# Kernel tuning notes

Hardware: AMD Instinct MI355X
Metric: run time of the kernel (lower is better)

The kernel has to match this reference:

```python
import jax, jax.numpy as jnp
import numpy as np

WS = (17, 5, 1)
NT = 23  # 17+5+1 tokens across levels
TABLE_ROWS = (2 * WS[0] - 1) * (2 * WS[0] - 1)  # 1089


def _rel_index():
    cs = []
    for i, w in enumerate(WS):
        c = np.arange(w, dtype=np.float32) - w // 2
        if i < len(WS) - 1:
            c = c * WS[0] / w  # rescale coarser levels to finest grid
        cs.append(c)
    c = np.concatenate(cs)  # [23]
    return (c[:, None] - c[None, :]) + (WS[0] - 1)  # [23,23] float

REL_IDX = jnp.asarray(_rel_index())


def _avgpool1d(x):
    # AvgPool1d(kernel=2, stride=2, padding=1, count_include_pad=False) on last axis (odd L)
    return jnp.concatenate([x[..., :1], (x[..., 1::2] + x[..., 2::2]) * 0.5], axis=-1)


def _l2norm(x):
    n = jnp.linalg.norm(x, axis=-1, keepdims=True)
    return x / jnp.maximum(n, 1e-12)


def _pos_embed(table, abs_bias):
    # table [1089,H], abs_bias [3,H,1,1,1] -> [1,H,1,23,23]
    idx = REL_IDX.reshape(-1)
    fl = jnp.clip(jnp.floor(idx), 0, TABLE_ROWS - 1).astype(jnp.int32)
    ce = jnp.clip(jnp.ceil(idx), 0, TABLE_ROWS - 1).astype(jnp.int32)
    w_ce = (idx - fl.astype(idx.dtype))[:, None]
    pe = (1.0 - w_ce) * table[fl] + w_ce * table[ce]  # [529,H]
    H = table.shape[1]
    pe = pe.reshape(1, 1, NT, NT, H).transpose(0, 4, 1, 2, 3)  # [1,H,1,23,23]
    chunks = jnp.split(pe, [WS[0], WS[0] + WS[1]], axis=3)
    chunks = [c + abs_bias[i][None] for i, c in enumerate(chunks)]
    return jnp.concatenate(chunks, axis=-2)


def _hifi(xh0, xh1, xh2, h_table, h_abs, h_proj_w, h_proj_b):
    q = jnp.concatenate([xh0[0], xh1[0], xh2[0]], axis=-2)  # [B,Hh,hd,23,S]
    k = jnp.concatenate([xh0[1], xh1[1], xh2[1]], axis=-2)
    v = jnp.concatenate([xh0[2], xh1[2], xh2[2]], axis=-2)
    attn = jnp.einsum('bhdts,bhdus->bhdtu', _l2norm(q), _l2norm(k))
    attn = attn + _pos_embed(h_table, h_abs)
    attn = jax.nn.softmax(attn, axis=-1)
    out = jnp.einsum('bhdtu,bhdus->bhdts', attn, v)
    return out @ h_proj_w.T + h_proj_b


def _lofi(xl0, xl1, xl2, l_table, l_abs, l_proj_w, l_proj_b):
    q = jnp.concatenate([xl0[0], xl1[0], xl2[0]], axis=-2)  # [B,Hl,hd,23,S]
    kvs = []
    for i, x in enumerate((xl0, xl1, xl2)):
        kv = x[1:]  # [2,B,Hl,hd,t_i,S]
        if i != 2:  # pool token axis for the two finer levels
            kv = jnp.moveaxis(_avgpool1d(jnp.moveaxis(kv, -2, -1)), -1, -2)
        kvs.append(kv)
    kv = jnp.concatenate(kvs, axis=-2)  # [2,B,Hl,hd,13,S]
    k, v = kv[0], kv[1]
    attn = jnp.einsum('bhdts,bhdus->bhdtu', _l2norm(q), _l2norm(k))  # [B,Hl,hd,23,13]
    pe = _pos_embed(l_table, l_abs)  # [1,Hl,1,23,23]
    Hl = l_table.shape[1]
    p1 = _avgpool1d(pe[..., :WS[0]].reshape(Hl, NT, WS[0])).reshape(1, Hl, 1, NT, -1)
    p2 = _avgpool1d(pe[..., WS[0]:WS[0] + WS[1]].reshape(Hl, NT, WS[1])).reshape(1, Hl, 1, NT, -1)
    p3 = pe[..., -1:]
    attn = attn + jnp.concatenate([p1, p2, p3], axis=-1)
    attn = jax.nn.softmax(attn, axis=-1)
    out = jnp.einsum('bhdtu,bhdus->bhdts', attn, v)
    return out @ l_proj_w.T + l_proj_b


def _forward(xh0, xh1, xh2, xl0, xl1, xl2, h_table, h_abs, l_table, l_abs,
             h_proj_w, h_proj_b, l_proj_w, l_proj_b):
    h_out = _hifi(xh0, xh1, xh2, h_table, h_abs, h_proj_w, h_proj_b)  # [B,1,64,23,S]
    l_out = _lofi(xl0, xl1, xl2, l_table, l_abs, l_proj_w, l_proj_b)  # [B,3,64,23,S]
    return jnp.concatenate([h_out, l_out], axis=1)  # [B,4,64,23,S]


def setup_inputs() -> dict:
    key = jax.random.key(0)
    ks = jax.random.split(key, 14)
    B, hd, S = 4, 64, 1024
    Hh, Hl = 1, 3
    d = {
        'xh0': jax.random.normal(ks[0], (3, B, Hh, hd, 17, S), jnp.float32),
        'xh1': jax.random.normal(ks[1], (3, B, Hh, hd, 5, S), jnp.float32),
        'xh2': jax.random.normal(ks[2], (3, B, Hh, hd, 1, S), jnp.float32),
        'xl0': jax.random.normal(ks[3], (3, B, Hl, hd, 17, S), jnp.float32),
        'xl1': jax.random.normal(ks[4], (3, B, Hl, hd, 5, S), jnp.float32),
        'xl2': jax.random.normal(ks[5], (3, B, Hl, hd, 1, S), jnp.float32),
        'h_table': jax.random.normal(ks[6], (TABLE_ROWS, Hh), jnp.float32) * 0.02,
        'h_abs': jax.random.normal(ks[7], (3, Hh, 1, 1, 1), jnp.float32) * 0.02,
        'l_table': jax.random.normal(ks[8], (TABLE_ROWS, Hl), jnp.float32) * 0.02,
        'l_abs': jax.random.normal(ks[9], (3, Hl, 1, 1, 1), jnp.float32) * 0.02,
        'h_proj_w': jax.random.normal(ks[10], (S, S), jnp.float32) / np.sqrt(S),
        'h_proj_b': jax.random.normal(ks[11], (S,), jnp.float32) * 0.01,
        'l_proj_w': jax.random.normal(ks[12], (S, S), jnp.float32) / np.sqrt(S),
        'l_proj_b': jax.random.normal(ks[13], (S,), jnp.float32) * 0.01,
    }
    return d


def reference(xh0, xh1, xh2, xl0, xl1, xl2, h_table, h_abs, l_table, l_abs,
              h_proj_w, h_proj_b, l_proj_w, l_proj_b):
    return _forward(xh0, xh1, xh2, xl0, xl1, xl2, h_table, h_abs, l_table, l_abs,
                    h_proj_w, h_proj_b, l_proj_w, l_proj_b)
```

## Files before the change

kernel.cpp:

```cpp
#include <hip/hip_runtime.h>
#include <hip/hip_bf16.h>
#include <stdint.h>

#define DEV __device__ __forceinline__

typedef float f32x4 __attribute__((ext_vector_type(4)));
typedef __bf16 bf16x8 __attribute__((ext_vector_type(8)));

DEV __bf16 tobf(float x){
  union { __hip_bfloat16 s; __bf16 b; } u; u.s = __float2bfloat16(x); return u.b;
}
DEV float bflo(uint32_t u){ return __uint_as_float(u << 16); }
DEV float bfhi(uint32_t u){ return __uint_as_float(u & 0xffff0000u); }
DEV float dot4(const float4& a, const float4& b){
  return a.x*b.x + a.y*b.y + a.z*b.z + a.w*b.w;
}
DEV bf16x8 pack8(const float4& a, const float4& b){
  bf16x8 r;
  r[0]=tobf(a.x); r[1]=tobf(a.y); r[2]=tobf(a.z); r[3]=tobf(a.w);
  r[4]=tobf(b.x); r[5]=tobf(b.y); r[6]=tobf(b.z); r[7]=tobf(b.w);
  return r;
}
DEV uint32_t f2bf2(float x, float y){
  union { __hip_bfloat16 b[2]; uint32_t u; } cv;
  cv.b[0] = __float2bfloat16(x); cv.b[1] = __float2bfloat16(y);
  return cv.u;
}
DEV float4 avg4(const float4& a, const float4& b){
  float4 r; r.x=0.5f*(a.x+b.x); r.y=0.5f*(a.y+b.y); r.z=0.5f*(a.z+b.z); r.w=0.5f*(a.w+b.w);
  return r;
}

DEV float relc(int j){
  if (j < 17) return (float)(j - 8);
  if (j < 22) return (float)(j - 19) * 3.4f;
  return 0.0f;
}
DEV int band_of(int t){ return t < 17 ? 0 : (t < 22 ? 1 : 2); }

template<int MODE> DEV void pool_map(int u, int& a, int& b){
  if (MODE == 0){ a = u; b = u; return; }
  if (u == 0){ a = 0; b = 0; }
  else if (u < 9){ a = 2*u - 1; b = 2*u; }
  else if (u == 9){ a = 17; b = 17; }
  else if (u < 12){ a = 2*u - 2; b = 2*u - 1; }
  else { a = 22; b = 22; }
}

DEV float interp_tab(const float* tab, int H, int h, int t, int u){
  float idx = relc(t) - relc(u) + 16.0f;
  float fl = floorf(idx);
  float ce = ceilf(idx);
  int fi = (int)fminf(fmaxf(fl, 0.f), 1088.f);
  int ci = (int)fminf(fmaxf(ce, 0.f), 1088.f);
  float w = idx - fl;
  return (1.0f - w) * tab[fi*H + h] + w * tab[ci*H + h];
}

template<int MODE>
DEV void qk_group(int gm, int qt,
    const float* __restrict__ x0, const float* __restrict__ x1, const float* __restrict__ x2,
    float* __restrict__ SpB,
    float* Spart , float* qnp , float* knp )
{
  constexpr int U = (MODE == 0) ? 23 : 13;
  constexpr int H = (MODE == 0) ? 1 : 3;
  int b, h, d;
  if (MODE == 0){ b = gm >> 6; h = 0; d = gm & 63; }
  else { b = gm / 192; int r = gm % 192; h = r >> 6; d = r & 63; }

  const int tid  = threadIdx.x;
  const int lane = tid & 63;
  const int w    = tid >> 6;
  const int lrow = lane & 15;
  const int kq   = lane >> 4;

  auto base_of = [&](int sel, int band) -> const float* {
    if (band == 0) return x0 + (size_t)((((sel*4 + b)*H + h)*64 + d)*17) * 1024;
    if (band == 1) return x1 + (size_t)((((sel*4 + b)*H + h)*64 + d)*5) * 1024;
    return x2 + (size_t)(((sel*4 + b)*H + h)*64 + d) * 1024;
  };
  const float* qb0 = base_of(0,0); const float* qb1 = base_of(0,1); const float* qb2 = base_of(0,2);
  const float* kb0 = base_of(1,0); const float* kb1 = base_of(1,1); const float* kb2 = base_of(1,2);

  auto rowp = [&](const float* r0, const float* r1, const float* r2, int t) -> const float* {
    if (t < 17) return r0 + (size_t)t * 1024;
    if (t < 22) return r1 + (size_t)(t - 17) * 1024;
    return r2;
  };

  const float* qr[2]; bool qv[2];
  #pragma unroll
  for (int mi = 0; mi < 2; ++mi){
    int t = mi*16 + lrow;
    qv[mi] = (t < 23);
    qr[mi] = qv[mi] ? rowp(qb0,qb1,qb2,t) : qb0;
  }
  const float* krA[2]; const float* krB[2]; bool kv[2];
  #pragma unroll
  for (int ni = 0; ni < 2; ++ni){
    int u = ni*16 + lrow;
    kv[ni] = (u < U);
    int au, bu; pool_map<MODE>(kv[ni] ? u : 0, au, bu);
    krA[ni] = rowp(kb0,kb1,kb2,au);
    krB[ni] = rowp(kb0,kb1,kb2,bu);
  }

  const int sbase = qt*256 + w*64 + kq*8;

  float4 qld[2][4];
  float4 kld[2][4];
  #pragma unroll
  for (int mi = 0; mi < 2; ++mi){
    #pragma unroll
    for (int kk = 0; kk < 2; ++kk){
      #pragma unroll
      for (int hf = 0; hf < 2; ++hf){
        qld[mi][kk*2+hf] = qv[mi] ? *(const float4*)(qr[mi] + sbase + kk*32 + hf*4)
                                  : float4{0,0,0,0};
      }
    }
  }
  if (MODE == 0){
    #pragma unroll
    for (int ni = 0; ni < 2; ++ni){
      #pragma unroll
      for (int kk = 0; kk < 2; ++kk){
        #pragma unroll
        for (int hf = 0; hf < 2; ++hf){
          kld[ni][kk*2+hf] = kv[ni] ? *(const float4*)(krA[ni] + sbase + kk*32 + hf*4)
                                    : float4{0,0,0,0};
        }
      }
    }
  } else {
    #pragma unroll
    for (int kk = 0; kk < 2; ++kk){
      #pragma unroll
      for (int hf = 0; hf < 2; ++hf){
        kld[0][kk*2+hf] = kv[0] ? *(const float4*)(krA[0] + sbase + kk*32 + hf*4)
                                : float4{0,0,0,0};
        kld[1][kk*2+hf] = kv[0] ? *(const float4*)(krB[0] + sbase + kk*32 + hf*4)
                                : float4{0,0,0,0};
      }
    }
  }

  f32x4 acc[2][2] = {};
  float qss[2] = {0.f, 0.f}, kss[2] = {0.f, 0.f};
  #pragma unroll
  for (int kk = 0; kk < 2; ++kk){
    bf16x8 qf[2], kf[2];
    #pragma unroll
    for (int mi = 0; mi < 2; ++mi){
      float4 v0 = qld[mi][kk*2], v1 = qld[mi][kk*2+1];
      qss[mi] += dot4(v0,v0) + dot4(v1,v1);
      qf[mi] = pack8(v0, v1);
    }
    if (MODE == 0){
      #pragma unroll
      for (int ni = 0; ni < 2; ++ni){
        float4 v0 = kld[ni][kk*2], v1 = kld[ni][kk*2+1];
        kss[ni] += dot4(v0,v0) + dot4(v1,v1);
        kf[ni] = pack8(v0, v1);
      }
    } else {
      float4 v0 = avg4(kld[0][kk*2], kld[1][kk*2]);
      float4 v1 = avg4(kld[0][kk*2+1], kld[1][kk*2+1]);
      kss[0] += dot4(v0,v0) + dot4(v1,v1);
      kf[0] = pack8(v0, v1);
    }
    #pragma unroll
    for (int mi = 0; mi < 2; ++mi){
      #pragma unroll
      for (int ni = 0; ni < 2; ++ni){
        if (MODE == 0 || ni == 0)
          acc[mi][ni] = __builtin_amdgcn_mfma_f32_16x16x32_bf16(qf[mi], kf[ni], acc[mi][ni], 0, 0, 0);
      }
    }
  }

  #pragma unroll
  for (int i = 0; i < 2; ++i){
    qss[i] += __shfl_xor(qss[i], 16); qss[i] += __shfl_xor(qss[i], 32);
    kss[i] += __shfl_xor(kss[i], 16); kss[i] += __shfl_xor(kss[i], 32);
  }
  if (lane < 16){
    qnp[w*32 + lane]      = qss[0];
    qnp[w*32 + 16 + lane] = qss[1];
    knp[w*32 + lane]      = kss[0];
    knp[w*32 + 16 + lane] = kss[1];
  }
  #pragma unroll
  for (int mi = 0; mi < 2; ++mi)
    #pragma unroll
    for (int ni = 0; ni < 2; ++ni)
      #pragma unroll
      for (int j = 0; j < 4; ++j)
        Spart[w*1056 + (mi*16 + kq*4 + j)*33 + ni*16 + lrow] = acc[mi][ni][j];
  __syncthreads();

  if (tid < 32){
    SpB[1024 + tid] = qnp[tid] + qnp[32+tid] + qnp[64+tid] + qnp[96+tid];
  } else if (tid < 64){
    int c = tid - 32;
    SpB[1056 + c] = knp[c] + knp[32+c] + knp[64+c] + knp[96+c];
  }
  {
    int r  = tid >> 3;
    int c0 = (tid & 7) * 4;
    float4 o;
    o.x = Spart[r*33+c0+0] + Spart[1056+r*33+c0+0] + Spart[2112+r*33+c0+0] + Spart[3168+r*33+c0+0];
    o.y = Spart[r*33+c0+1] + Spart[1056+r*33+c0+1] + Spart[2112+r*33+c0+1] + Spart[3168+r*33+c0+1];
    o.z = Spart[r*33+c0+2] + Spart[1056+r*33+c0+2] + Spart[2112+r*33+c0+2] + Spart[3168+r*33+c0+2];
    o.w = Spart[r*33+c0+3] + Spart[1056+r*33+c0+3] + Spart[2112+r*33+c0+3] + Spart[3168+r*33+c0+3];
    *(float4*)(SpB + r*32 + c0) = o;
  }
}

__global__ __launch_bounds__(256, 4) void fused_a(
    const float* __restrict__ xh0, const float* __restrict__ xh1, const float* __restrict__ xh2,
    const float* __restrict__ xl0, const float* __restrict__ xl1, const float* __restrict__ xl2,
    const float* __restrict__ htab, const float* __restrict__ habs,
    const float* __restrict__ ltab, const float* __restrict__ labs,
    const float* __restrict__ hw, const float* __restrict__ lw,
    float* __restrict__ Sp, __hip_bfloat16* __restrict__ Vb,
    float* __restrict__ pe_h, float* __restrict__ pe_l,
    __hip_bfloat16* __restrict__ whb, __hip_bfloat16* __restrict__ wlb)
{
  __shared__ __align__(16) float Spart[4*32*33];
  __shared__ float qnp[4*32], knp[4*32];
  const int bid = blockIdx.x;
  const int tid = threadIdx.x;

  if (bid < 4096){
    int g = bid >> 2, qt = bid & 3;
    float* SpB = Sp + (size_t)bid * 1088;
    if (g < 256) qk_group<0>(g,       qt, xh0, xh1, xh2, SpB, Spart, qnp, knp);
    else         qk_group<1>(g - 256, qt, xl0, xl1, xl2, SpB, Spart, qnp, knp);
    return;
  }

  if (bid < 6080){
    const int vb_ = bid - 4096;
    auto vsrc = [&](int r, const float*& pa, const float*& pb){
      if (r < 5888){
        int gg = r / 23, u = r - gg*23;
        int b = gg >> 6, d = gg & 63;
        const float* v0 = xh0 + (size_t)(((8 + b)*64 + d)*17) * 1024;
        const float* v1 = xh1 + (size_t)(((8 + b)*64 + d)*5) * 1024;
        const float* v2 = xh2 + (size_t)((8 + b)*64 + d) * 1024;
        pa = (u < 17) ? v0 + (size_t)u*1024 : (u < 22 ? v1 + (size_t)(u-17)*1024 : v2);
        pb = pa;
      } else {
        int rr = r - 5888;
        int gm = rr / 13, u = rr - gm*13;
        int b = gm / 192, rem = gm % 192, h = rem >> 6, d = rem & 63;
        const float* v0 = xl0 + (size_t)((((8 + b)*3 + h)*64 + d)*17) * 1024;
        const float* v1 = xl1 + (size_t)((((8 + b)*3 + h)*64 + d)*5) * 1024;
        const float* v2 = xl2 + (size_t)(((8 + b)*3 + h)*64 + d) * 1024;
        int au, bu; pool_map<1>(u, au, bu);
        pa = (au < 17) ? v0 + (size_t)au*1024 : (au < 22 ? v1 + (size_t)(au-17)*1024 : v2);
        pb = (bu < 17) ? v0 + (size_t)bu*1024 : (bu < 22 ? v1 + (size_t)(bu-17)*1024 : v2);
      }
    };
    const int c0 = tid * 4;
    float4 va[8], vbv[8]; bool two[8];
    #pragma unroll
    for (int i = 0; i < 8; ++i){
      int r = vb_*8 + i;
      const float *pa, *pb; vsrc(r, pa, pb);
      va[i] = *(const float4*)(pa + c0);
      two[i] = (pb != pa);
      vbv[i] = two[i] ? *(const float4*)(pb + c0) : va[i];
    }
    #pragma unroll
    for (int i = 0; i < 8; ++i){
      float4 a = two[i] ? avg4(va[i], vbv[i]) : va[i];
      uint2 o; o.x = f2bf2(a.x, a.y); o.y = f2bf2(a.z, a.w);
      *(uint2*)(Vb + (size_t)(vb_*8 + i)*1024 + c0) = o;
    }
    return;
  }

  const int pb_ = bid - 6080;
  if (pb_ < 1024){
    int i = (pb_*256 + tid)*8;
    const float* src; __hip_bfloat16* dst;
    if (i < 1048576){ src = hw + i; dst = whb + i; }
    else { src = lw + (i - 1048576); dst = wlb + (i - 1048576); }
    float4 x0 = *(const float4*)(src);
    float4 x1 = *(const float4*)(src + 4);
    uint4 o;
    o.x = f2bf2(x0.x, x0.y); o.y = f2bf2(x0.z, x0.w);
    o.z = f2bf2(x1.x, x1.y); o.w = f2bf2(x1.z, x1.w);
    *(uint4*)dst = o;
  } else if (pb_ == 1024){
    for (int j = tid; j < 529; j += 256){
      int t = j / 23, u = j % 23;
      pe_h[j] = interp_tab(htab, 1, 0, t, u) + habs[band_of(t)];
    }
  } else {
    for (int j = tid; j < 897; j += 256){
      int h = j / 299, r = j % 299, t = r / 13, u = r % 13;
      int a, b; pool_map<1>(u, a, b);
      pe_l[j] = 0.5f * (interp_tab(ltab, 3, h, t, a) + interp_tab(ltab, 3, h, t, b))
              + labs[band_of(t)*3 + h];
    }
  }
}

__global__ __launch_bounds__(256) void gemm_vw(
    const __hip_bfloat16* __restrict__ A,
    const __hip_bfloat16* __restrict__ Wh, const __hip_bfloat16* __restrict__ Wl,
    __hip_bfloat16* __restrict__ VW)
{
  __shared__ __hip_bfloat16 lA[2][128*64];
  __shared__ __hip_bfloat16 lB[2][128*64];
  const int tid  = threadIdx.x;
  const int lane = tid & 63;

  const int bid = blockIdx.x;
  const int swz = (bid & 7) * 124 + (bid >> 3);
  const int mt = swz >> 3, nt = swz & 7;
  const int tM = mt * 128, tN = nt * 128;
  const bool hifi = (mt < 46);
  const __hip_bfloat16* W = hifi ? Wh : Wl;

  const int wm = ((tid >> 6) >> 1) * 64, wn = ((tid >> 6) & 1) * 64;
  f32x4 acc[4][4] = {};

  const int srow = tid >> 3;
  const int scol = ((tid & 7) * 8) ^ ((srow & 7) * 8);
  const __hip_bfloat16* ga = A + (size_t)(tM + srow) * 1024 + scol;
  const __hip_bfloat16* gb = W + (size_t)(tN + srow) * 1024 + scol;

  auto stage = [&](int buf, int k0){
    #pragma unroll
    for (int q = 0; q < 4; ++q){
      __builtin_amdgcn_global_load_lds(
        (const __attribute__((address_space(1))) void*)(ga + k0 + (size_t)q*32*1024),
        (__attribute__((address_space(3))) void*)(&lA[buf][q*2048 + tid*8]), 16, 0, 0);
      __builtin_amdgcn_global_load_lds(
        (const __attribute__((address_space(1))) void*)(gb + k0 + (size_t)q*32*1024),
        (__attribute__((address_space(3))) void*)(&lB[buf][q*2048 + tid*8]), 16, 0, 0);
    }
  };

  const int rsw = (lane & 7) * 8;
  auto compute = [&](int buf){
    #pragma unroll
    for (int kk = 0; kk < 2; ++kk){
      const int cb = (kk*32 + (lane >> 4)*8) ^ rsw;
      bf16x8 af[4], bfr[4];
      #pragma unroll
      for (int mi = 0; mi < 4; ++mi)
        af[mi] = *(const bf16x8*)(&lA[buf][(wm + mi*16 + (lane & 15))*64 + cb]);
      #pragma unroll
      for (int ni = 0; ni < 4; ++ni)
        bfr[ni] = *(const bf16x8*)(&lB[buf][(wn + ni*16 + (lane & 15))*64 + cb]);
      #pragma unroll
      for (int mi = 0; mi < 4; ++mi){
        #pragma unroll
        for (int ni = 0; ni < 4; ++ni)
          acc[mi][ni] = __builtin_amdgcn_mfma_f32_16x16x32_bf16(af[mi], bfr[ni], acc[mi][ni], 0, 0, 0);
      }
    }
  };

  stage(0, 0);
  __syncthreads();
  int cur = 0;
  #pragma unroll 1
  for (int t = 0; t < 15; ++t){
    stage(cur ^ 1, (t + 1) * 64);
    compute(cur);
    __syncthreads();
    cur ^= 1;
  }
  compute(cur);

  #pragma unroll
  for (int mi = 0; mi < 4; ++mi){
    #pragma unroll
    for (int j = 0; j < 4; ++j){
      int r = tM + wm + mi*16 + (lane >> 4)*4 + j;
      __hip_bfloat16* po = VW + (size_t)r * 1024 + tN + wn + (lane & 15);
      #pragma unroll
      for (int ni = 0; ni < 4; ++ni)
        po[ni*16] = __float2bfloat16(acc[mi][ni][j]);
    }
  }
}

template<int MODE>
DEV void mix_group(int g, int sh, int tid,
    const float* __restrict__ Sp, const float* __restrict__ pe,
    const __hip_bfloat16* __restrict__ VW, const float* __restrict__ bias,
    float* __restrict__ out, float* lds_p)
{
  constexpr int U  = (MODE == 0) ? 23 : 13;
  constexpr int UP = (MODE == 0) ? 24 : 16;
  int gm = (MODE == 0) ? g : g - 256;
  int b, h, d;
  if (MODE == 0){ b = gm >> 6; h = 0; d = gm & 63; }
  else { b = gm / 192; int rem = gm % 192; h = rem >> 6; d = rem & 63; }

  {
    int r = tid >> 3, c0 = (tid & 7) * 4;
    const float* A0 = Sp + (size_t)(4*g) * 1088;
    const float* A1 = A0 + 1088;
    const float* A2 = A0 + 2176;
    const float* A3 = A0 + 3264;
    float qn = A0[1024 + r] + A1[1024 + r] + A2[1024 + r] + A3[1024 + r];
    float iqn = 1.0f / fmaxf(sqrtf(qn), 1e-12f);
    float vals[4];
    #pragma unroll
    for (int j = 0; j < 4; ++j){
      int c = c0 + j;
      bool valid = (r < 23) && (c < U);
      if (valid){
        float sv = A0[r*32 + c] + A1[r*32 + c] + A2[r*32 + c] + A3[r*32 + c];
        float kn = A0[1056 + c] + A1[1056 + c] + A2[1056 + c] + A3[1056 + c];
        float ikn = 1.0f / fmaxf(sqrtf(kn), 1e-12f);
        float pv = (MODE == 0) ? pe[r*23 + c] : pe[(h*23 + r)*13 + c];
        vals[j] = sv * iqn * ikn + pv;
      } else vals[j] = -3.0e38f;
    }
    float m = fmaxf(fmaxf(vals[0], vals[1]), fmaxf(vals[2], vals[3]));
    m = fmaxf(m, __shfl_xor(m, 1)); m = fmaxf(m, __shfl_xor(m, 2)); m = fmaxf(m, __shfl_xor(m, 4));
    float e[4], ssum = 0.f;
    #pragma unroll
    for (int j = 0; j < 4; ++j){ e[j] = __expf(vals[j] - m); ssum += e[j]; }
    ssum += __shfl_xor(ssum, 1); ssum += __shfl_xor(ssum, 2); ssum += __shfl_xor(ssum, 4);
    float inv = 1.0f / ssum;
    if (r < 23){
      #pragma unroll
      for (int j = 0; j < 4; ++j)
        lds_p[r*32 + c0 + j] = (c0 + j < U) ? e[j] * inv : 0.f;
    }
  }
  __syncthreads();

  const int s0 = sh*512 + tid*2;
  const uint16_t* vwb = (const uint16_t*)VW +
      ((MODE == 0) ? (size_t)g*23*1024 : (size_t)(5888 + gm*13)*1024) + s0;
  float2 vv[UP];
  #pragma unroll
  for (int u = 0; u < UP; ++u){
    if (u < U){
      uint32_t w2 = *(const uint32_t*)(vwb + (size_t)u*1024);
      vv[u].x = bflo(w2); vv[u].y = bfhi(w2);
    } else { vv[u].x = 0.f; vv[u].y = 0.f; }
  }
  const float bx = bias[s0], by = bias[s0 + 1];
  const int orow0 = (MODE == 0) ? (b*5888 + d*23) : (b*5888 + (1 + h)*1472 + d*23);

  #pragma unroll 2
  for (int t = 0; t < 23; ++t){
    float ax = bx, ay = by;
    #pragma unroll
    for (int u4 = 0; u4 < UP/4; ++u4){
      float4 p = *(const float4*)(lds_p + t*32 + u4*4);
      ax += p.x*vv[u4*4+0].x + p.y*vv[u4*4+1].x + p.z*vv[u4*4+2].x + p.w*vv[u4*4+3].x;
      ay += p.x*vv[u4*4+0].y + p.y*vv[u4*4+1].y + p.z*vv[u4*4+2].y + p.w*vv[u4*4+3].y;
    }
    float2 o2; o2.x = ax; o2.y = ay;
    *(float2*)(out + (size_t)(orow0 + t)*1024 + s0) = o2;
  }
}

__global__ __launch_bounds__(256) void mix_all(
    const float* __restrict__ Sp, const float* __restrict__ pe_h, const float* __restrict__ pe_l,
    const __hip_bfloat16* __restrict__ VW,
    const float* __restrict__ hb, const float* __restrict__ lb,
    float* __restrict__ out)
{
  __shared__ __align__(16) float lds_p[23*32];
  int bid = blockIdx.x;
  int g = bid >> 1, sh = bid & 1;
  if (g < 256) mix_group<0>(g, sh, threadIdx.x, Sp, pe_h, VW, hb, out, lds_p);
  else         mix_group<1>(g, sh, threadIdx.x, Sp, pe_l, VW, lb, out, lds_p);
}

extern "C" void kernel_launch(void* const* d_in, const int* in_sizes, int n_in,
                              void* d_out, int out_size, void* d_ws, size_t ws_size,
                              hipStream_t stream) {
  const float* xh0  = (const float*)d_in[0];
  const float* xh1  = (const float*)d_in[1];
  const float* xh2  = (const float*)d_in[2];
  const float* xl0  = (const float*)d_in[3];
  const float* xl1  = (const float*)d_in[4];
  const float* xl2  = (const float*)d_in[5];
  const float* htab = (const float*)d_in[6];
  const float* habs = (const float*)d_in[7];
  const float* ltab = (const float*)d_in[8];
  const float* labs = (const float*)d_in[9];
  const float* hw   = (const float*)d_in[10];
  const float* hb   = (const float*)d_in[11];
  const float* lw   = (const float*)d_in[12];
  const float* lb   = (const float*)d_in[13];
  float* out = (float*)d_out;

  char* ws = (char*)d_ws;
  float* pe_h = (float*)ws;
  float* pe_l = (float*)(ws + 2176);
  __hip_bfloat16* VW  = (__hip_bfloat16*)(ws + 8192);
  float* Sp           = (float*)(ws + 8192 + 32505856);

  __hip_bfloat16* Vb  = (__hip_bfloat16*)out;
  __hip_bfloat16* whb = (__hip_bfloat16*)(out + 23068672);
  __hip_bfloat16* wlb = whb + 1048576;

  fused_a<<<7106, 256, 0, stream>>>(xh0, xh1, xh2, xl0, xl1, xl2,
                                    htab, habs, ltab, labs, hw, lw,
                                    Sp, Vb, pe_h, pe_l, whb, wlb);
  gemm_vw<<<992, 256, 0, stream>>>(Vb, whb, wlb, VW);
  mix_all<<<2048, 256, 0, stream>>>(Sp, pe_h, pe_l, VW, hb, lb, out);
}
```

Before: 155.3 us.

## Replace VW GEMM with 256x256-tile 8-wave kernel using phased async loads

After: 159.7 us. +2.8%, slower.

```diff
diff --git a/kernel.cpp b/kernel.cpp
--- a/kernel.cpp
+++ b/kernel.cpp
@@ -310,85 +310,136 @@
   }
 }
 
-__global__ __launch_bounds__(256) void gemm_vw(
+template<int N> DEV void vwait(){ asm volatile("s_waitcnt vmcnt(%0)" :: "n"(N) : "memory"); }
+
+__global__ __launch_bounds__(512, 2) void gemm8(
     const __hip_bfloat16* __restrict__ A,
     const __hip_bfloat16* __restrict__ Wh, const __hip_bfloat16* __restrict__ Wl,
     __hip_bfloat16* __restrict__ VW)
 {
-  __shared__ __hip_bfloat16 lA[2][128*64];
-  __shared__ __hip_bfloat16 lB[2][128*64];
+  __shared__ __hip_bfloat16 lA[2][2][128*64];
+  __shared__ __hip_bfloat16 lB[2][2][128*64];
   const int tid  = threadIdx.x;
   const int lane = tid & 63;
+  const int mw = (tid >> 6) >> 2;
+  const int nw = (tid >> 6) & 3;
 
   const int bid = blockIdx.x;
-  const int swz = (bid & 7) * 124 + (bid >> 3);
-  const int mt = swz >> 3, nt = swz & 7;
-  const int tM = mt * 128, tN = nt * 128;
-  const bool hifi = (mt < 46);
-  const __hip_bfloat16* W = hifi ? Wh : Wl;
-
-  const int wm = ((tid >> 6) >> 1) * 64, wn = ((tid >> 6) & 1) * 64;
-  f32x4 acc[4][4] = {};
+  const int swz = (bid & 7) * 31 + (bid >> 3);
+  const int mt = swz >> 2, nt = swz & 3;
+  const int tM = mt * 256, tN = nt * 256;
+  const __hip_bfloat16* W = (mt < 23) ? Wh : Wl;
 
   const int srow = tid >> 3;
-  const int scol = ((tid & 7) * 8) ^ ((srow & 7) * 8);
-  const __hip_bfloat16* ga = A + (size_t)(tM + srow) * 1024 + scol;
-  const __hip_bfloat16* gb = W + (size_t)(tN + srow) * 1024 + scol;
-
-  auto stage = [&](int buf, int k0){
-    #pragma unroll
-    for (int q = 0; q < 4; ++q){
+  const int schunk = tid & 7;
+
+  auto stageA = [&](int par, int ht, int t){
+    #pragma unroll
+    for (int r = 0; r < 2; ++r){
+      int ri = r*64 + srow;
+      int grow = tM + ht*128 + ri;
+      int gcol = t*64 + ((schunk ^ (ri & 7)) * 8);
       __builtin_amdgcn_global_load_lds(
-        (const __attribute__((address_space(1))) void*)(ga + k0 + (size_t)q*32*1024),
-        (__attribute__((address_space(3))) void*)(&lA[buf][q*2048 + tid*8]), 16, 0, 0);
+        (const __attribute__((address_space(1))) void*)(A + (size_t)grow*1024 + gcol),
+        (__attribute__((address_space(3))) void*)(&lA[par][ht][ri*64 + schunk*8]), 16, 0, 0);
+    }
+  };
+  auto stageB = [&](int par, int ht, int t){
+    #pragma unroll
+    for (int r = 0; r < 2; ++r){
+      int ri = r*64 + srow;
+      int grow = tN + ht*128 + ri;
+      int gcol = t*64 + ((schunk ^ (ri & 7)) * 8);
       __builtin_amdgcn_global_load_lds(
-        (const __attribute__((address_space(1))) void*)(gb + k0 + (size_t)q*32*1024),
-        (__attribute__((address_space(3))) void*)(&lB[buf][q*2048 + tid*8]), 16, 0, 0);
+        (const __attribute__((address_space(1))) void*)(W + (size_t)grow*1024 + gcol),
+        (__attribute__((address_space(3))) void*)(&lB[par][ht][ri*64 + schunk*8]), 16, 0, 0);
     }
   };
 
-  const int rsw = (lane & 7) * 8;
-  auto compute = [&](int buf){
-    #pragma unroll
-    for (int kk = 0; kk < 2; ++kk){
-      const int cb = (kk*32 + (lane >> 4)*8) ^ rsw;
-      bf16x8 af[4], bfr[4];
-      #pragma unroll
-      for (int mi = 0; mi < 4; ++mi)
-        af[mi] = *(const bf16x8*)(&lA[buf][(wm + mi*16 + (lane & 15))*64 + cb]);
-      #pragma unroll
-      for (int ni = 0; ni < 4; ++ni)
-        bfr[ni] = *(const bf16x8*)(&lB[buf][(wn + ni*16 + (lane & 15))*64 + cb]);
-      #pragma unroll
-      for (int mi = 0; mi < 4; ++mi){
+  f32x4 acc[2][2][4][2] = {};
+
+  auto phase_mfma = [&](int par, int mh, int nh){
+    bf16x8 af[4][2], bf_[2][2];
+    #pragma unroll
+    for (int fi = 0; fi < 4; ++fi){
+      #pragma unroll
+      for (int kk = 0; kk < 2; ++kk){
+        int ri = mw*64 + fi*16 + (lane & 15);
+        int c  = (kk*32 + (lane >> 4)*8) ^ ((ri & 7)*8);
+        af[fi][kk] = *(const bf16x8*)(&lA[par][mh][ri*64 + c]);
+      }
+    }
+    #pragma unroll
+    for (int fj = 0; fj < 2; ++fj){
+      #pragma unroll
+      for (int kk = 0; kk < 2; ++kk){
+        int ri = nw*32 + fj*16 + (lane & 15);
+        int c  = (kk*32 + (lane >> 4)*8) ^ ((ri & 7)*8);
+        bf_[fj][kk] = *(const bf16x8*)(&lB[par][nh][ri*64 + c]);
+      }
+    }
+    __builtin_amdgcn_s_barrier();
+    __builtin_amdgcn_s_setprio(1);
+    #pragma unroll
+    for (int fi = 0; fi < 4; ++fi){
+      #pragma unroll
+      for (int fj = 0; fj < 2; ++fj){
         #pragma unroll
-        for (int ni = 0; ni < 4; ++ni)
-          acc[mi][ni] = __builtin_amdgcn_mfma_f32_16x16x32_bf16(af[mi], bfr[ni], acc[mi][ni], 0, 0, 0);
-      }
-    }
+        for (int kk = 0; kk < 2; ++kk){
+          f32x4* pacc = &acc[0][0][0][0] + ((mh*2 + nh)*4 + fi)*2 + fj;
+          *pacc = __builtin_amdgcn_mfma_f32_16x16x32_bf16(af[fi][kk], bf_[fj][kk], *pacc, 0, 0, 0);
+        }
+      }
+    }
+    __builtin_amdgcn_s_setprio(0);
+    __builtin_amdgcn_s_barrier();
   };
 
-  stage(0, 0);
-  __syncthreads();
-  int cur = 0;
+  stageA(0, 0, 0); stageB(0, 0, 0); stageB(0, 1, 0); stageA(0, 1, 0);
+  stageA(1, 0, 1); stageB(1, 0, 1);
+
   #pragma unroll 1
   for (int t = 0; t < 15; ++t){
-    stage(cur ^ 1, (t + 1) * 64);
-    compute(cur);
-    __syncthreads();
-    cur ^= 1;
-  }
-  compute(cur);
-
-  #pragma unroll
-  for (int mi = 0; mi < 4; ++mi){
-    #pragma unroll
-    for (int j = 0; j < 4; ++j){
-      int r = tM + wm + mi*16 + (lane >> 4)*4 + j;
-      __hip_bfloat16* po = VW + (size_t)r * 1024 + tN + wn + (lane & 15);
-      #pragma unroll
-      for (int ni = 0; ni < 4; ++ni)
-        po[ni*16] = __float2bfloat16(acc[mi][ni][j]);
+    const int par = t & 1;
+    vwait<8>();
+    { bf16x8 dummy; (void)dummy; }
+    stageB(par ^ 1, 1, t + 1);
+    phase_mfma(par, 0, 0);
+    vwait<8>();
+    stageA(par ^ 1, 1, t + 1);
+    phase_mfma(par, 0, 1);
+    vwait<8>();
+    if (t + 2 <= 15) stageA(par, 0, t + 2);
+    phase_mfma(par, 1, 0);
+    if (t + 2 <= 15) stageB(par, 0, t + 2);
+    phase_mfma(par, 1, 1);
+  }
+  {
+    vwait<4>();
+    phase_mfma(1, 0, 0);
+    vwait<2>();
+    phase_mfma(1, 0, 1);
+    vwait<0>();
+    phase_mfma(1, 1, 0);
+    phase_mfma(1, 1, 1);
+  }
+
+  #pragma unroll
+  for (int mh = 0; mh < 2; ++mh){
+    #pragma unroll
+    for (int nh = 0; nh < 2; ++nh){
+      #pragma unroll
+      for (int fi = 0; fi < 4; ++fi){
+        #pragma unroll
+        for (int fj = 0; fj < 2; ++fj){
+          #pragma unroll
+          for (int j = 0; j < 4; ++j){
+            int row = tM + mh*128 + mw*64 + fi*16 + (lane >> 4)*4 + j;
+            int col = tN + nh*128 + nw*32 + fj*16 + (lane & 15);
+            VW[(size_t)row * 1024 + col] = __float2bfloat16(acc[mh][nh][fi][fj][j]);
+          }
+        }
+      }
     }
   }
 }
@@ -515,6 +566,6 @@
   fused_a<<<7106, 256, 0, stream>>>(xh0, xh1, xh2, xl0, xl1, xl2,
                                     htab, habs, ltab, labs, hw, lw,
                                     Sp, Vb, pe_h, pe_l, whb, wlb);
-  gemm_vw<<<992, 256, 0, stream>>>(Vb, whb, wlb, VW);
+  gemm8<<<248, 512, 0, stream>>>(Vb, whb, wlb, VW);
   mix_all<<<2048, 256, 0, stream>>>(Sp, pe_h, pe_l, VW, hb, lb, out);
 }
```

## Stage Q/K as bf16 in a relayout pass and fuse softmax into a QK kernel

Applied to the files above, without the earlier changes.

New measurement: 179.2 us. 1.15x slower.

```diff
diff --git a/kernel.cpp b/kernel.cpp
--- a/kernel.cpp
+++ b/kernel.cpp
@@ -7,20 +7,8 @@
 typedef float f32x4 __attribute__((ext_vector_type(4)));
 typedef __bf16 bf16x8 __attribute__((ext_vector_type(8)));
 
-DEV __bf16 tobf(float x){
-  union { __hip_bfloat16 s; __bf16 b; } u; u.s = __float2bfloat16(x); return u.b;
-}
 DEV float bflo(uint32_t u){ return __uint_as_float(u << 16); }
 DEV float bfhi(uint32_t u){ return __uint_as_float(u & 0xffff0000u); }
-DEV float dot4(const float4& a, const float4& b){
-  return a.x*b.x + a.y*b.y + a.z*b.z + a.w*b.w;
-}
-DEV bf16x8 pack8(const float4& a, const float4& b){
-  bf16x8 r;
-  r[0]=tobf(a.x); r[1]=tobf(a.y); r[2]=tobf(a.z); r[3]=tobf(a.w);
-  r[4]=tobf(b.x); r[5]=tobf(b.y); r[6]=tobf(b.z); r[7]=tobf(b.w);
-  return r;
-}
 DEV uint32_t f2bf2(float x, float y){
   union { __hip_bfloat16 b[2]; uint32_t u; } cv;
   cv.b[0] = __float2bfloat16(x); cv.b[1] = __float2bfloat16(y);
@@ -30,6 +18,21 @@
   float4 r; r.x=0.5f*(a.x+b.x); r.y=0.5f*(a.y+b.y); r.z=0.5f*(a.z+b.z); r.w=0.5f*(a.w+b.w);
   return r;
 }
+DEV bf16x8 ldz(const __hip_bfloat16* p, bool valid){
+  if (valid) return *(const bf16x8*)p;
+  bf16x8 z = {};
+  return z;
+}
+DEV float sumsq8(bf16x8 v){
+  union { bf16x8 b; uint32_t u[4]; } cv; cv.b = v;
+  float s = 0.f;
+  #pragma unroll
+  for (int i = 0; i < 4; ++i){
+    float a = bflo(cv.u[i]), b = bfhi(cv.u[i]);
+    s += a*a + b*b;
+  }
+  return s;
+}
 
 DEV float relc(int j){
   if (j < 17) return (float)(j - 8);
@@ -38,8 +41,7 @@
 }
 DEV int band_of(int t){ return t < 17 ? 0 : (t < 22 ? 1 : 2); }
 
-template<int MODE> DEV void pool_map(int u, int& a, int& b){
-  if (MODE == 0){ a = u; b = u; return; }
+DEV void pool_map1(int u, int& a, int& b){
   if (u == 0){ a = 0; b = 0; }
   else if (u < 9){ a = 2*u - 1; b = 2*u; }
   else if (u == 9){ a = 17; b = 17; }
@@ -57,235 +59,129 @@
   return (1.0f - w) * tab[fi*H + h] + w * tab[ci*H + h];
 }
 
-template<int MODE>
-DEV void qk_group(int gm, int qt,
-    const float* __restrict__ x0, const float* __restrict__ x1, const float* __restrict__ x2,
-    float* __restrict__ SpB,
-    float* Spart , float* qnp , float* knp )
-{
-  constexpr int U = (MODE == 0) ? 23 : 13;
-  constexpr int H = (MODE == 0) ? 1 : 3;
-  int b, h, d;
-  if (MODE == 0){ b = gm >> 6; h = 0; d = gm & 63; }
-  else { b = gm / 192; int r = gm % 192; h = r >> 6; d = r & 63; }
-
-  const int tid  = threadIdx.x;
-  const int lane = tid & 63;
-  const int w    = tid >> 6;
-  const int lrow = lane & 15;
-  const int kq   = lane >> 4;
-
-  auto base_of = [&](int sel, int band) -> const float* {
-    if (band == 0) return x0 + (size_t)((((sel*4 + b)*H + h)*64 + d)*17) * 1024;
-    if (band == 1) return x1 + (size_t)((((sel*4 + b)*H + h)*64 + d)*5) * 1024;
-    return x2 + (size_t)(((sel*4 + b)*H + h)*64 + d) * 1024;
-  };
-  const float* qb0 = base_of(0,0); const float* qb1 = base_of(0,1); const float* qb2 = base_of(0,2);
-  const float* kb0 = base_of(1,0); const float* kb1 = base_of(1,1); const float* kb2 = base_of(1,2);
-
-  auto rowp = [&](const float* r0, const float* r1, const float* r2, int t) -> const float* {
-    if (t < 17) return r0 + (size_t)t * 1024;
-    if (t < 22) return r1 + (size_t)(t - 17) * 1024;
-    return r2;
-  };
-
-  const float* qr[2]; bool qv[2];
-  #pragma unroll
-  for (int mi = 0; mi < 2; ++mi){
-    int t = mi*16 + lrow;
-    qv[mi] = (t < 23);
-    qr[mi] = qv[mi] ? rowp(qb0,qb1,qb2,t) : qb0;
-  }
-  const float* krA[2]; const float* krB[2]; bool kv[2];
-  #pragma unroll
-  for (int ni = 0; ni < 2; ++ni){
-    int u = ni*16 + lrow;
-    kv[ni] = (u < U);
-    int au, bu; pool_map<MODE>(kv[ni] ? u : 0, au, bu);
-    krA[ni] = rowp(kb0,kb1,kb2,au);
-    krB[ni] = rowp(kb0,kb1,kb2,bu);
-  }
-
-  const int sbase = qt*256 + w*64 + kq*8;
-
-  float4 qld[2][4];
-  float4 kld[2][4];
-  #pragma unroll
-  for (int mi = 0; mi < 2; ++mi){
-    #pragma unroll
-    for (int kk = 0; kk < 2; ++kk){
-      #pragma unroll
-      for (int hf = 0; hf < 2; ++hf){
-        qld[mi][kk*2+hf] = qv[mi] ? *(const float4*)(qr[mi] + sbase + kk*32 + hf*4)
-                                  : float4{0,0,0,0};
-      }
-    }
-  }
-  if (MODE == 0){
-    #pragma unroll
-    for (int ni = 0; ni < 2; ++ni){
-      #pragma unroll
-      for (int kk = 0; kk < 2; ++kk){
-        #pragma unroll
-        for (int hf = 0; hf < 2; ++hf){
-          kld[ni][kk*2+hf] = kv[ni] ? *(const float4*)(krA[ni] + sbase + kk*32 + hf*4)
-                                    : float4{0,0,0,0};
-        }
-      }
-    }
+DEV const float* qk_src(int SEL, bool hif, int gm, int u,
+    const float* xh0, const float* xh1, const float* xh2,
+    const float* xl0, const float* xl1, const float* xl2)
+{
+  if (hif){
+    int b = gm >> 6, d = gm & 63;
+    size_t base = (size_t)((SEL*4 + b)*64 + d);
+    if (u < 17) return xh0 + (base*17 + u) * 1024;
+    if (u < 22) return xh1 + (base*5 + (u - 17)) * 1024;
+    return xh2 + base * 1024;
   } else {
-    #pragma unroll
-    for (int kk = 0; kk < 2; ++kk){
-      #pragma unroll
-      for (int hf = 0; hf < 2; ++hf){
-        kld[0][kk*2+hf] = kv[0] ? *(const float4*)(krA[0] + sbase + kk*32 + hf*4)
-                                : float4{0,0,0,0};
-        kld[1][kk*2+hf] = kv[0] ? *(const float4*)(krB[0] + sbase + kk*32 + hf*4)
-                                : float4{0,0,0,0};
-      }
-    }
-  }
-
-  f32x4 acc[2][2] = {};
-  float qss[2] = {0.f, 0.f}, kss[2] = {0.f, 0.f};
-  #pragma unroll
-  for (int kk = 0; kk < 2; ++kk){
-    bf16x8 qf[2], kf[2];
-    #pragma unroll
-    for (int mi = 0; mi < 2; ++mi){
-      float4 v0 = qld[mi][kk*2], v1 = qld[mi][kk*2+1];
-      qss[mi] += dot4(v0,v0) + dot4(v1,v1);
-      qf[mi] = pack8(v0, v1);
-    }
-    if (MODE == 0){
-      #pragma unroll
-      for (int ni = 0; ni < 2; ++ni){
-        float4 v0 = kld[ni][kk*2], v1 = kld[ni][kk*2+1];
-        kss[ni] += dot4(v0,v0) + dot4(v1,v1);
-        kf[ni] = pack8(v0, v1);
-      }
-    } else {
-      float4 v0 = avg4(kld[0][kk*2], kld[1][kk*2]);
-      float4 v1 = avg4(kld[0][kk*2+1], kld[1][kk*2+1]);
-      kss[0] += dot4(v0,v0) + dot4(v1,v1);
-      kf[0] = pack8(v0, v1);
-    }
-    #pragma unroll
-    for (int mi = 0; mi < 2; ++mi){
-      #pragma unroll
-      for (int ni = 0; ni < 2; ++ni){
-        if (MODE == 0 || ni == 0)
-          acc[mi][ni] = __builtin_amdgcn_mfma_f32_16x16x32_bf16(qf[mi], kf[ni], acc[mi][ni], 0, 0, 0);
-      }
-    }
-  }
-
-  #pragma unroll
-  for (int i = 0; i < 2; ++i){
-    qss[i] += __shfl_xor(qss[i], 16); qss[i] += __shfl_xor(qss[i], 32);
-    kss[i] += __shfl_xor(kss[i], 16); kss[i] += __shfl_xor(kss[i], 32);
-  }
-  if (lane < 16){
-    qnp[w*32 + lane]      = qss[0];
-    qnp[w*32 + 16 + lane] = qss[1];
-    knp[w*32 + lane]      = kss[0];
-    knp[w*32 + 16 + lane] = kss[1];
-  }
-  #pragma unroll
-  for (int mi = 0; mi < 2; ++mi)
-    #pragma unroll
-    for (int ni = 0; ni < 2; ++ni)
-      #pragma unroll
-      for (int j = 0; j < 4; ++j)
-        Spart[w*1056 + (mi*16 + kq*4 + j)*33 + ni*16 + lrow] = acc[mi][ni][j];
-  __syncthreads();
-
-  if (tid < 32){
-    SpB[1024 + tid] = qnp[tid] + qnp[32+tid] + qnp[64+tid] + qnp[96+tid];
-  } else if (tid < 64){
-    int c = tid - 32;
-    SpB[1056 + c] = knp[c] + knp[32+c] + knp[64+c] + knp[96+c];
-  }
-  {
-    int r  = tid >> 3;
-    int c0 = (tid & 7) * 4;
-    float4 o;
-    o.x = Spart[r*33+c0+0] + Spart[1056+r*33+c0+0] + Spart[2112+r*33+c0+0] + Spart[3168+r*33+c0+0];
-    o.y = Spart[r*33+c0+1] + Spart[1056+r*33+c0+1] + Spart[2112+r*33+c0+1] + Spart[3168+r*33+c0+1];
-    o.z = Spart[r*33+c0+2] + Spart[1056+r*33+c0+2] + Spart[2112+r*33+c0+2] + Spart[3168+r*33+c0+2];
-    o.w = Spart[r*33+c0+3] + Spart[1056+r*33+c0+3] + Spart[2112+r*33+c0+3] + Spart[3168+r*33+c0+3];
-    *(float4*)(SpB + r*32 + c0) = o;
-  }
-}
-
-__global__ __launch_bounds__(256, 4) void fused_a(
+    int b = gm / 192, rem = gm % 192, h = rem >> 6, d = rem & 63;
+    size_t base = (size_t)(((SEL*4 + b)*3 + h)*64 + d);
+    if (u < 17) return xl0 + (base*17 + u) * 1024;
+    if (u < 22) return xl1 + (base*5 + (u - 17)) * 1024;
+    return xl2 + base * 1024;
+  }
+}
+
+__global__ __launch_bounds__(256, 4) void relayout(
     const float* __restrict__ xh0, const float* __restrict__ xh1, const float* __restrict__ xh2,
     const float* __restrict__ xl0, const float* __restrict__ xl1, const float* __restrict__ xl2,
     const float* __restrict__ htab, const float* __restrict__ habs,
     const float* __restrict__ ltab, const float* __restrict__ labs,
     const float* __restrict__ hw, const float* __restrict__ lw,
-    float* __restrict__ Sp, __hip_bfloat16* __restrict__ Vb,
-    float* __restrict__ pe_h, float* __restrict__ pe_l,
-    __hip_bfloat16* __restrict__ whb, __hip_bfloat16* __restrict__ wlb)
-{
-  __shared__ __align__(16) float Spart[4*32*33];
-  __shared__ float qnp[4*32], knp[4*32];
-  const int bid = blockIdx.x;
-  const int tid = threadIdx.x;
-
-  if (bid < 4096){
-    int g = bid >> 2, qt = bid & 3;
-    float* SpB = Sp + (size_t)bid * 1088;
-    if (g < 256) qk_group<0>(g,       qt, xh0, xh1, xh2, SpB, Spart, qnp, knp);
-    else         qk_group<1>(g - 256, qt, xl0, xl1, xl2, SpB, Spart, qnp, knp);
+    __hip_bfloat16* __restrict__ Qh, __hip_bfloat16* __restrict__ Ql,
+    __hip_bfloat16* __restrict__ Kh, __hip_bfloat16* __restrict__ Kl,
+    __hip_bfloat16* __restrict__ Vb,
+    __hip_bfloat16* __restrict__ whb, __hip_bfloat16* __restrict__ wlb,
+    float* __restrict__ pe_h, float* __restrict__ pe_l)
+{
+  const int bid = blockIdx.x, tid = threadIdx.x;
+  const int c0 = tid * 4;
+
+  if (bid < 2944){
+    const int r0 = bid * 8;
+    float4 va[8];
+    #pragma unroll
+    for (int i = 0; i < 8; ++i){
+      int r = r0 + i;
+      bool hif = (r < 5888);
+      int rr = hif ? r : r - 5888;
+      const float* s = qk_src(0, hif, rr / 23, rr % 23, xh0,xh1,xh2,xl0,xl1,xl2);
+      va[i] = *(const float4*)(s + c0);
+    }
+    #pragma unroll
+    for (int i = 0; i < 8; ++i){
+      int r = r0 + i;
+      bool hif = (r < 5888);
+      int rr = hif ? r : r - 5888;
+      __hip_bfloat16* dst = (hif ? Qh : Ql) + (size_t)rr * 1024;
+      uint2 o; o.x = f2bf2(va[i].x, va[i].y); o.y = f2bf2(va[i].z, va[i].w);
+      *(uint2*)(dst + c0) = o;
+    }
     return;
   }
 
-  if (bid < 6080){
-    const int vb_ = bid - 4096;
-    auto vsrc = [&](int r, const float*& pa, const float*& pb){
+  if (bid < 3680){
+    const int r0 = (bid - 2944) * 8;
+    float4 va[8];
+    #pragma unroll
+    for (int i = 0; i < 8; ++i){
+      int r = r0 + i;
+      const float* s = qk_src(1, true, r / 23, r % 23, xh0,xh1,xh2,xl0,xl1,xl2);
+      va[i] = *(const float4*)(s + c0);
+    }
+    #pragma unroll
+    for (int i = 0; i < 8; ++i){
+      int r = r0 + i;
+      uint2 o; o.x = f2bf2(va[i].x, va[i].y); o.y = f2bf2(va[i].z, va[i].w);
+      *(uint2*)(Kh + (size_t)r * 1024 + c0) = o;
+    }
+    return;
+  }
+
+  if (bid < 4928){
+    const int rr0 = (bid - 3680) * 8;
+    float4 va[8], vb[8];
+    #pragma unroll
+    for (int i = 0; i < 8; ++i){
+      int rr = rr0 + i;
+      int gm = rr / 13, u = rr % 13;
+      int au, bu; pool_map1(u, au, bu);
+      va[i] = *(const float4*)(qk_src(1, false, gm, au, xh0,xh1,xh2,xl0,xl1,xl2) + c0);
+      vb[i] = (bu != au) ? *(const float4*)(qk_src(1, false, gm, bu, xh0,xh1,xh2,xl0,xl1,xl2) + c0) : va[i];
+    }
+    #pragma unroll
+    for (int i = 0; i < 8; ++i){
+      float4 a = avg4(va[i], vb[i]);
+      uint2 o; o.x = f2bf2(a.x, a.y); o.y = f2bf2(a.z, a.w);
+      *(uint2*)(Kl + (size_t)(rr0 + i) * 1024 + c0) = o;
+    }
+    return;
+  }
+
+  if (bid < 6912){
+    const int r0 = (bid - 4928) * 8;
+    float4 va[8], vb[8];
+    #pragma unroll
+    for (int i = 0; i < 8; ++i){
+      int r = r0 + i;
       if (r < 5888){
-        int gg = r / 23, u = r - gg*23;
-        int b = gg >> 6, d = gg & 63;
-        const float* v0 = xh0 + (size_t)(((8 + b)*64 + d)*17) * 1024;
-        const float* v1 = xh1 + (size_t)(((8 + b)*64 + d)*5) * 1024;
-        const float* v2 = xh2 + (size_t)((8 + b)*64 + d) * 1024;
-        pa = (u < 17) ? v0 + (size_t)u*1024 : (u < 22 ? v1 + (size_t)(u-17)*1024 : v2);
-        pb = pa;
+        va[i] = *(const float4*)(qk_src(2, true, r / 23, r % 23, xh0,xh1,xh2,xl0,xl1,xl2) + c0);
+        vb[i] = va[i];
       } else {
         int rr = r - 5888;
-        int gm = rr / 13, u = rr - gm*13;
-        int b = gm / 192, rem = gm % 192, h = rem >> 6, d = rem & 63;
-        const float* v0 = xl0 + (size_t)((((8 + b)*3 + h)*64 + d)*17) * 1024;
-        const float* v1 = xl1 + (size_t)((((8 + b)*3 + h)*64 + d)*5) * 1024;
-        const float* v2 = xl2 + (size_t)(((8 + b)*3 + h)*64 + d) * 1024;
-        int au, bu; pool_map<1>(u, au, bu);
-        pa = (au < 17) ? v0 + (size_t)au*1024 : (au < 22 ? v1 + (size_t)(au-17)*1024 : v2);
-        pb = (bu < 17) ? v0 + (size_t)bu*1024 : (bu < 22 ? v1 + (size_t)(bu-17)*1024 : v2);
+        int gm = rr / 13, u = rr % 13;
+        int au, bu; pool_map1(u, au, bu);
+        va[i] = *(const float4*)(qk_src(2, false, gm, au, xh0,xh1,xh2,xl0,xl1,xl2) + c0);
+        vb[i] = (bu != au) ? *(const float4*)(qk_src(2, false, gm, bu, xh0,xh1,xh2,xl0,xl1,xl2) + c0) : va[i];
       }
-    };
-    const int c0 = tid * 4;
-    float4 va[8], vbv[8]; bool two[8];
-    #pragma unroll
-    for (int i = 0; i < 8; ++i){
-      int r = vb_*8 + i;
-      const float *pa, *pb; vsrc(r, pa, pb);
-      va[i] = *(const float4*)(pa + c0);
-      two[i] = (pb != pa);
-      vbv[i] = two[i] ? *(const float4*)(pb + c0) : va[i];
-    }
-    #pragma unroll
-    for (int i = 0; i < 8; ++i){
-      float4 a = two[i] ? avg4(va[i], vbv[i]) : va[i];
+    }
+    #pragma unroll
+    for (int i = 0; i < 8; ++i){
+      float4 a = avg4(va[i], vb[i]);
       uint2 o; o.x = f2bf2(a.x, a.y); o.y = f2bf2(a.z, a.w);
-      *(uint2*)(Vb + (size_t)(vb_*8 + i)*1024 + c0) = o;
+      *(uint2*)(Vb + (size_t)(r0 + i) * 1024 + c0) = o;
     }
     return;
   }
 
-  const int pb_ = bid - 6080;
-  if (pb_ < 1024){
-    int i = (pb_*256 + tid)*8;
+  if (bid < 7936){
+    int i = ((bid - 6912)*256 + tid)*8;
     const float* src; __hip_bfloat16* dst;
     if (i < 1048576){ src = hw + i; dst = whb + i; }
     else { src = lw + (i - 1048576); dst = wlb + (i - 1048576); }
@@ -295,7 +191,10 @@
     o.x = f2bf2(x0.x, x0.y); o.y = f2bf2(x0.z, x0.w);
     o.z = f2bf2(x1.x, x1.y); o.w = f2bf2(x1.z, x1.w);
     *(uint4*)dst = o;
-  } else if (pb_ == 1024){
+    return;
+  }
+
+  if (bid == 7936){
     for (int j = tid; j < 529; j += 256){
       int t = j / 23, u = j % 23;
       pe_h[j] = interp_tab(htab, 1, 0, t, u) + habs[band_of(t)];
@@ -303,13 +202,145 @@
   } else {
     for (int j = tid; j < 897; j += 256){
       int h = j / 299, r = j % 299, t = r / 13, u = r % 13;
-      int a, b; pool_map<1>(u, a, b);
+      int a, b; pool_map1(u, a, b);
       pe_l[j] = 0.5f * (interp_tab(ltab, 3, h, t, a) + interp_tab(ltab, 3, h, t, b))
               + labs[band_of(t)*3 + h];
     }
   }
 }
 
+template<int MODE>
+DEV void qkp_group(int gidx, int gm,
+    const __hip_bfloat16* __restrict__ Qg, const __hip_bfloat16* __restrict__ Kg,
+    const float* __restrict__ pe, float* __restrict__ P,
+    float* Spart, float* qnp, float* knp, float* iqn_l, float* ikn_l)
+{
+  constexpr int U = (MODE == 0) ? 23 : 13;
+  const int h = (MODE == 0) ? 0 : ((gm % 192) >> 6);
+  const int tid  = threadIdx.x;
+  const int lane = tid & 63;
+  const int w    = tid >> 6;
+  const int lrow = lane & 15;
+  const int kq   = lane >> 4;
+
+  f32x4 acc[2][2] = {};
+  float qss[2] = {0.f, 0.f}, kss[2] = {0.f, 0.f};
+  const int cbase = w*256 + kq*8;
+
+  #pragma unroll
+  for (int kk = 0; kk < 8; ++kk){
+    const int scol = cbase + kk*32;
+    bf16x8 qf[2], kf[2];
+    #pragma unroll
+    for (int mi = 0; mi < 2; ++mi){
+      int row = mi*16 + lrow;
+      qf[mi] = ldz(Qg + (size_t)row*1024 + scol, row < 23);
+      qss[mi] += sumsq8(qf[mi]);
+    }
+    if (MODE == 0){
+      #pragma unroll
+      for (int ni = 0; ni < 2; ++ni){
+        int row = ni*16 + lrow;
+        kf[ni] = ldz(Kg + (size_t)row*1024 + scol, row < 23);
+        kss[ni] += sumsq8(kf[ni]);
+      }
+    } else {
+      kf[0] = ldz(Kg + (size_t)lrow*1024 + scol, lrow < 13);
+      kss[0] += sumsq8(kf[0]);
+      kf[1] = kf[0];
+    }
+    #pragma unroll
+    for (int mi = 0; mi < 2; ++mi){
+      #pragma unroll
+      for (int ni = 0; ni < 2; ++ni){
+        if (MODE == 0 || ni == 0)
+          acc[mi][ni] = __builtin_amdgcn_mfma_f32_16x16x32_bf16(qf[mi], kf[ni], acc[mi][ni], 0, 0, 0);
+      }
+    }
+  }
+
+  #pragma unroll
+  for (int i = 0; i < 2; ++i){
+    qss[i] += __shfl_xor(qss[i], 16); qss[i] += __shfl_xor(qss[i], 32);
+    kss[i] += __shfl_xor(kss[i], 16); kss[i] += __shfl_xor(kss[i], 32);
+  }
+  if (lane < 16){
+    qnp[w*32 + lane]      = qss[0];
+    qnp[w*32 + 16 + lane] = qss[1];
+    knp[w*32 + lane]      = kss[0];
+    knp[w*32 + 16 + lane] = kss[1];
+  }
+  #pragma unroll
+  for (int mi = 0; mi < 2; ++mi)
+    #pragma unroll
+    for (int ni = 0; ni < 2; ++ni)
+      #pragma unroll
+      for (int j = 0; j < 4; ++j)
+        Spart[w*1056 + (mi*16 + kq*4 + j)*33 + ni*16 + lrow] = acc[mi][ni][j];
+  __syncthreads();
+
+  if (tid < 32){
+    float s = qnp[tid] + qnp[32+tid] + qnp[64+tid] + qnp[96+tid];
+    iqn_l[tid] = 1.0f / fmaxf(sqrtf(s), 1e-12f);
+  } else if (tid < 64){
+    int c = tid - 32;
+    float s = knp[c] + knp[32+c] + knp[64+c] + knp[96+c];
+    ikn_l[c] = 1.0f / fmaxf(sqrtf(s), 1e-12f);
+  }
+  __syncthreads();
+
+  {
+    int r  = tid >> 3;
+    int c0 = (tid & 7) * 4;
+    float aiq = iqn_l[r & 31];
+    float vals[4];
+    #pragma unroll
+    for (int j = 0; j < 4; ++j){
+      int c = c0 + j;
+      bool valid = (r < 23) && (c < U);
+      if (valid){
+        float sv = Spart[r*33 + c] + Spart[1056 + r*33 + c] + Spart[2112 + r*33 + c] + Spart[3168 + r*33 + c];
+        float pv = (MODE == 0) ? pe[r*23 + c] : pe[(h*23 + r)*13 + c];
+        vals[j] = sv * aiq * ikn_l[c] + pv;
+      } else vals[j] = -3.0e38f;
+    }
+    float m = fmaxf(fmaxf(vals[0], vals[1]), fmaxf(vals[2], vals[3]));
+    m = fmaxf(m, __shfl_xor(m, 1)); m = fmaxf(m, __shfl_xor(m, 2)); m = fmaxf(m, __shfl_xor(m, 4));
+    float e[4], ssum = 0.f;
+    #pragma unroll
+    for (int j = 0; j < 4; ++j){ e[j] = __expf(vals[j] - m); ssum += e[j]; }
+    ssum += __shfl_xor(ssum, 1); ssum += __shfl_xor(ssum, 2); ssum += __shfl_xor(ssum, 4);
+    float inv = 1.0f / ssum;
+    if (r < 23){
+      #pragma unroll
+      for (int j = 0; j < 4; ++j){
+        int c = c0 + j;
+        P[(size_t)gidx*736 + r*32 + c] = (c < U) ? e[j] * inv : 0.f;
+      }
+    }
+  }
+}
+
+__global__ __launch_bounds__(256) void qkp_kernel(
+    const __hip_bfloat16* __restrict__ Qh, const __hip_bfloat16* __restrict__ Ql,
+    const __hip_bfloat16* __restrict__ Kh, const __hip_bfloat16* __restrict__ Kl,
+    const float* __restrict__ pe_h, const float* __restrict__ pe_l,
+    float* __restrict__ P)
+{
+  __shared__ __align__(16) float Spart[4*32*33];
+  __shared__ float qnp[128], knp[128], iqn_l[32], ikn_l[32];
+  int g = blockIdx.x;
+  if (g < 256){
+    qkp_group<0>(g, g, Qh + (size_t)g*23552, Kh + (size_t)g*23552,
+                 pe_h, P, Spart, qnp, knp, iqn_l, ikn_l);
+  } else {
+    int gm = g - 256;
+    qkp_group<1>(g, gm, Ql + (size_t)gm*23552, Kl + (size_t)gm*13312,
+                 pe_l, P, Spart, qnp, knp, iqn_l, ikn_l);
+  }
+}
+
+typedef __bf16 bf16x8_t __attribute__((ext_vector_type(8)));
 __global__ __launch_bounds__(256) void gemm_vw(
     const __hip_bfloat16* __restrict__ A,
     const __hip_bfloat16* __restrict__ Wh, const __hip_bfloat16* __restrict__ Wl,
@@ -395,7 +426,7 @@
 
 template<int MODE>
 DEV void mix_group(int g, int sh, int tid,
-    const float* __restrict__ Sp, const float* __restrict__ pe,
+    const float* __restrict__ P,
     const __hip_bfloat16* __restrict__ VW, const float* __restrict__ bias,
     float* __restrict__ out, float* lds_p)
 {
@@ -406,40 +437,7 @@
   if (MODE == 0){ b = gm >> 6; h = 0; d = gm & 63; }
   else { b = gm / 192; int rem = gm % 192; h = rem >> 6; d = rem & 63; }
 
-  {
-    int r = tid >> 3, c0 = (tid & 7) * 4;
-    const float* A0 = Sp + (size_t)(4*g) * 1088;
-    const float* A1 = A0 + 1088;
-    const float* A2 = A0 + 2176;
-    const float* A3 = A0 + 3264;
-    float qn = A0[1024 + r] + A1[1024 + r] + A2[1024 + r] + A3[1024 + r];
-    float iqn = 1.0f / fmaxf(sqrtf(qn), 1e-12f);
-    float vals[4];
-    #pragma unroll
-    for (int j = 0; j < 4; ++j){
-      int c = c0 + j;
-      bool valid = (r < 23) && (c < U);
-      if (valid){
-        float sv = A0[r*32 + c] + A1[r*32 + c] + A2[r*32 + c] + A3[r*32 + c];
-        float kn = A0[1056 + c] + A1[1056 + c] + A2[1056 + c] + A3[1056 + c];
-        float ikn = 1.0f / fmaxf(sqrtf(kn), 1e-12f);
-        float pv = (MODE == 0) ? pe[r*23 + c] : pe[(h*23 + r)*13 + c];
-        vals[j] = sv * iqn * ikn + pv;
-      } else vals[j] = -3.0e38f;
-    }
-    float m = fmaxf(fmaxf(vals[0], vals[1]), fmaxf(vals[2], vals[3]));
-    m = fmaxf(m, __shfl_xor(m, 1)); m = fmaxf(m, __shfl_xor(m, 2)); m = fmaxf(m, __shfl_xor(m, 4));
-    float e[4], ssum = 0.f;
-    #pragma unroll
-    for (int j = 0; j < 4; ++j){ e[j] = __expf(vals[j] - m); ssum += e[j]; }
-    ssum += __shfl_xor(ssum, 1); ssum += __shfl_xor(ssum, 2); ssum += __shfl_xor(ssum, 4);
-    float inv = 1.0f / ssum;
-    if (r < 23){
-      #pragma unroll
-      for (int j = 0; j < 4; ++j)
-        lds_p[r*32 + c0 + j] = (c0 + j < U) ? e[j] * inv : 0.f;
-    }
-  }
+  if (tid < 184) ((float4*)lds_p)[tid] = ((const float4*)(P + (size_t)g*736))[tid];
   __syncthreads();
 
   const int s0 = sh*512 + tid*2;
@@ -471,7 +469,7 @@
 }
 
 __global__ __launch_bounds__(256) void mix_all(
-    const float* __restrict__ Sp, const float* __restrict__ pe_h, const float* __restrict__ pe_l,
+    const float* __restrict__ P,
     const __hip_bfloat16* __restrict__ VW,
     const float* __restrict__ hb, const float* __restrict__ lb,
     float* __restrict__ out)
@@ -479,8 +477,8 @@
   __shared__ __align__(16) float lds_p[23*32];
   int bid = blockIdx.x;
   int g = bid >> 1, sh = bid & 1;
-  if (g < 256) mix_group<0>(g, sh, threadIdx.x, Sp, pe_h, VW, hb, out, lds_p);
-  else         mix_group<1>(g, sh, threadIdx.x, Sp, pe_l, VW, lb, out, lds_p);
+  if (g < 256) mix_group<0>(g, sh, threadIdx.x, P, VW, hb, out, lds_p);
+  else         mix_group<1>(g, sh, threadIdx.x, P, VW, lb, out, lds_p);
 }
 
 extern "C" void kernel_launch(void* const* d_in, const int* in_sizes, int n_in,
@@ -505,16 +503,21 @@
   char* ws = (char*)d_ws;
   float* pe_h = (float*)ws;
   float* pe_l = (float*)(ws + 2176);
-  __hip_bfloat16* VW  = (__hip_bfloat16*)(ws + 8192);
-  float* Sp           = (float*)(ws + 8192 + 32505856);
+  __hip_bfloat16* VW = (__hip_bfloat16*)(ws + 8192);
+  __hip_bfloat16* Kh = (__hip_bfloat16*)(ws + 8192);
+  __hip_bfloat16* Kl = Kh + (size_t)5888 * 1024;
+  float* P = (float*)(ws + 8192 + 32505856);
 
   __hip_bfloat16* Vb  = (__hip_bfloat16*)out;
+  __hip_bfloat16* Qh  = (__hip_bfloat16*)((char*)out + 32505856);
+  __hip_bfloat16* Ql  = Qh + (size_t)5888 * 1024;
   __hip_bfloat16* whb = (__hip_bfloat16*)(out + 23068672);
   __hip_bfloat16* wlb = whb + 1048576;
 
-  fused_a<<<7106, 256, 0, stream>>>(xh0, xh1, xh2, xl0, xl1, xl2,
-                                    htab, habs, ltab, labs, hw, lw,
-                                    Sp, Vb, pe_h, pe_l, whb, wlb);
+  relayout<<<7938, 256, 0, stream>>>(xh0, xh1, xh2, xl0, xl1, xl2,
+                                     htab, habs, ltab, labs, hw, lw,
+                                     Qh, Ql, Kh, Kl, Vb, whb, wlb, pe_h, pe_l);
+  qkp_kernel<<<1024, 256, 0, stream>>>(Qh, Ql, Kh, Kl, pe_h, pe_l, P);
   gemm_vw<<<992, 256, 0, stream>>>(Vb, whb, wlb, VW);
-  mix_all<<<2048, 256, 0, stream>>>(Sp, pe_h, pe_l, VW, hb, lb, out);
-}
+  mix_all<<<2048, 256, 0, stream>>>(P, VW, hb, lb, out);
+}
```
